# Optimization experiments

Measured on AMD Instinct MI355X. Metric: run time of the kernel, lower is better.

Reference implementation:

```python
import jax, jax.numpy as jnp
import numpy as np

B, LQ, LV = 32, 64, 128
QS, FS, BN = 512, 1024, 512

def setup_inputs() -> dict:
    key = jax.random.key(0)
    k1, k2, k3, k4, k5 = jax.random.split(key, 5)
    s = lambda n: 1.0 / np.sqrt(n)
    return {
        "phr_feats": jax.random.normal(k1, (B, LQ, QS), dtype=jnp.float32),
        "vis_feats": jax.random.normal(k2, (B, LV, FS), dtype=jnp.float32),
        "W": jax.random.uniform(k3, (BN, QS), jnp.float32, -s(QS), s(QS)),
        "U": jax.random.uniform(k4, (BN, FS), jnp.float32, -s(FS), s(FS)),
        "b": jnp.ones((BN,), dtype=jnp.float32),
        "w": jax.random.uniform(k5, (1, BN), jnp.float32, -s(BN), s(BN)),
    }

def reference(phr_feats, vis_feats, W, U, b, w):
    # Wh: [B,Lq,BN], Uv: [B,Lv,BN]
    Wh = jnp.einsum('bqd,nd->bqn', phr_feats, W)
    Uv = jnp.einsum('bvf,nf->bvn', vis_feats, U)
    # broadcast add + tanh: [B,Lq,Lv,BN]
    t = jnp.tanh(Wh[:, :, None, :] + Uv[:, None, :, :] + b)
    energies = jnp.einsum('bqvn,n->bqv', t, w[0])  # squeeze(-1)
    weights = jax.nn.softmax(energies, axis=2)
    aligned = jnp.einsum('bqv,bvf->bqf', weights, vis_feats)
    semantic_group_feats = jnp.concatenate([phr_feats, aligned], axis=2)
    return (semantic_group_feats, weights, energies)
```

## Files before the change

### kernel.cpp

```cpp
#include <hip/hip_runtime.h>

#define NB  32
#define NLQ 64
#define NLV 128
#define NQS 512
#define NFS 1024
#define NBN 512
#define CC  2.8853900817779268f

typedef float  floatx4 __attribute__((ext_vector_type(4)));
typedef __bf16 bf16x8  __attribute__((ext_vector_type(8)));
typedef unsigned short us;

__device__ __forceinline__ us f2bf(float f) {
    unsigned int u = __float_as_uint(f);
    u += 0x7fffu + ((u >> 16) & 1u);
    return (us)(u >> 16);
}
__device__ __forceinline__ unsigned int pktrunc(float lo, float hi) {
    return __builtin_amdgcn_perm(__float_as_uint(hi), __float_as_uint(lo), 0x07060302u);
}
__device__ __forceinline__ float blo(unsigned int u) {
    return __uint_as_float(u << 16);
}
__device__ __forceinline__ float bhi(unsigned int u) {
    return __uint_as_float(u & 0xffff0000u);
}

__device__ __forceinline__ void gemm64(
    us* As, us* Bs,
    const float* __restrict__ A, const float* __restrict__ Bt,
    const float* __restrict__ bias,
    float* __restrict__ whYp, us* __restrict__ uvYTp,
    int K, int bx, int by,
    float* __restrict__ sgf, us* __restrict__ visbT)
{
    const int tid  = threadIdx.x;
    const int m0   = bx * 64;
    const int n0   = by * 64;
    const int wave = tid >> 6;
    const int lane = tid & 63;
    const int wm   = (wave >> 1) * 32;
    const int wn   = (wave & 1) * 32;
    const int srow = tid >> 2;
    const int sk   = (tid & 3) * 8;
    const int fm   = lane & 15;
    const int fko  = (lane >> 4) * 8;

    floatx4 acc[2][2] = {};
    const float* ag = A  + (size_t)(m0 + srow) * K + sk;
    const float* bg = Bt + (size_t)(n0 + srow) * K + sk;

    float4 a0 = *(const float4*)(ag),     a1 = *(const float4*)(ag + 4);
    float4 b0 = *(const float4*)(bg),     b1 = *(const float4*)(bg + 4);

    for (int k0 = 0; k0 < K; k0 += 32) {
        __syncthreads();
        if (sgf) {
            float* d = sgf + (size_t)(m0 + srow) * (NQS + NFS) + k0 + sk;
            *(float4*)d       = a0;
            *(float4*)(d + 4) = a1;
        }
        uint4 av = { pktrunc(a0.x, a0.y), pktrunc(a0.z, a0.w),
                     pktrunc(a1.x, a1.y), pktrunc(a1.z, a1.w) };
        uint4 bv = { pktrunc(b0.x, b0.y), pktrunc(b0.z, b0.w),
                     pktrunc(b1.x, b1.y), pktrunc(b1.z, b1.w) };
        *(uint4*)(As + srow * 40 + sk) = av;
        *(uint4*)(Bs + srow * 40 + sk) = bv;
        const int kn = k0 + 32;
        if (kn < K) {
            a0 = *(const float4*)(ag + kn); a1 = *(const float4*)(ag + kn + 4);
            b0 = *(const float4*)(bg + kn); b1 = *(const float4*)(bg + kn + 4);
        }
        __syncthreads();
        bf16x8 am[2], bn[2];
        #pragma unroll
        for (int i = 0; i < 2; ++i)
            am[i] = *(const bf16x8*)(As + (wm + 16 * i + fm) * 40 + fko);
        #pragma unroll
        for (int j = 0; j < 2; ++j)
            bn[j] = *(const bf16x8*)(Bs + (wn + 16 * j + fm) * 40 + fko);
        #pragma unroll
        for (int i = 0; i < 2; ++i)
            #pragma unroll
            for (int j = 0; j < 2; ++j)
                acc[i][j] = __builtin_amdgcn_mfma_f32_16x16x32_bf16(am[i], bn[j], acc[i][j], 0, 0, 0);

        if (visbT) {
            const int bb = m0 >> 7, vbase = m0 & 127;
            #pragma unroll
            for (int h = 0; h < 2; ++h) {
                int idx = h * 256 + tid;
                int f   = idx >> 4;
                int v0  = (idx & 15) * 4;
                us e0 = As[(v0 + 0) * 40 + f];
                us e1 = As[(v0 + 1) * 40 + f];
                us e2 = As[(v0 + 2) * 40 + f];
                us e3 = As[(v0 + 3) * 40 + f];
                uint2 pk2 = { (unsigned int)e0 | ((unsigned int)e1 << 16),
                              (unsigned int)e2 | ((unsigned int)e3 << 16) };
                *(uint2*)(visbT + ((size_t)bb * NFS + k0 + f) * NLV + vbase + v0) = pk2;
            }
        }
    }

    const int cr = (lane >> 4) * 4;
    const int cc = lane & 15;
    if (whYp) {
        #pragma unroll
        for (int i = 0; i < 2; ++i)
            #pragma unroll
            for (int j = 0; j < 2; ++j)
                #pragma unroll
                for (int r = 0; r < 4; ++r) {
                    int gm = m0 + wm + 16 * i + cr + r;
                    int gn = n0 + wn + 16 * j + cc;
                    float v = acc[i][j][r] + bias[gn];
                    whYp[(size_t)gm * NBN + gn] = __builtin_amdgcn_exp2f(CC * v);
                }
    } else {
        #pragma unroll
        for (int i = 0; i < 2; ++i)
            #pragma unroll
            for (int j = 0; j < 2; ++j) {
                int gm0 = m0 + wm + 16 * i + cr;
                int gn  = n0 + wn + 16 * j + cc;
                int bb  = gm0 >> 7, v = gm0 & 127;
                unsigned int y0 = f2bf(__builtin_amdgcn_exp2f(CC * acc[i][j][0]));
                unsigned int y1 = f2bf(__builtin_amdgcn_exp2f(CC * acc[i][j][1]));
                unsigned int y2 = f2bf(__builtin_amdgcn_exp2f(CC * acc[i][j][2]));
                unsigned int y3 = f2bf(__builtin_amdgcn_exp2f(CC * acc[i][j][3]));
                uint2 pk2 = { y0 | (y1 << 16), y2 | (y3 << 16) };
                *(uint2*)(uvYTp + ((size_t)bb * NBN + gn) * NLV + v) = pk2;
            }
    }
}

__global__ __launch_bounds__(256) void gemm_both(
    const float* __restrict__ phr, const float* __restrict__ W,
    const float* __restrict__ bias,
    const float* __restrict__ vis, const float* __restrict__ U,
    float* __restrict__ whY, us* __restrict__ uvYT,
    float* __restrict__ out_sgf, us* __restrict__ visbT)
{
    __shared__ __align__(16) us As[64 * 40];
    __shared__ __align__(16) us Bs[64 * 40];
    int blk = blockIdx.x;
    if (blk < 256) {
        int bx = blk % 32, by = blk / 32;
        gemm64(As, Bs, phr, W, bias, whY, nullptr, NQS, bx, by,
               by == 0 ? out_sgf : nullptr, nullptr);
    } else {
        blk -= 256;
        int bx = blk % 64, by = blk / 64;
        gemm64(As, Bs, vis, U, bias, nullptr, uvYT, NFS, bx, by,
               nullptr, by == 0 ? visbT : nullptr);
    }
}

__global__ __launch_bounds__(256) void energize(
    const float* __restrict__ whY,
    const us* __restrict__ uvYT,
    const float* __restrict__ wvec,
    float* __restrict__ out_w, float* __restrict__ out_e,
    us* __restrict__ p_bf, us* __restrict__ p_lo)
{
    const float LOG2E = 1.4426950408889634f;
    int blk = blockIdx.x;
    blk = (blk & 7) * 64 + (blk >> 3);
    const int b    = blk >> 4;
    const int qq4  = blk & 15;
    const int tid  = threadIdx.x;
    const int wave = __builtin_amdgcn_readfirstlane(tid >> 6);
    const int lane = tid & 63;
    const int q0   = qq4 * 4;

    __shared__ float part[4][4][NLV];

    float4 sw0 = *(const float4*)(wvec + lane * 8);
    float4 sw1 = *(const float4*)(wvec + lane * 8 + 4);
    float sumw = sw0.x + sw0.y + sw0.z + sw0.w + sw1.x + sw1.y + sw1.z + sw1.w;
    #pragma unroll
    for (int off = 32; off; off >>= 1) sumw += __shfl_xor(sumw, off);

    const float* yqp = whY + (size_t)(b * NLQ + q0) * NBN + wave * 128;
    const float* wp  = wvec + wave * 128;
    const us*    uvp = uvYT + ((size_t)b * NBN + wave * 128) * NLV + 2 * lane;

    float acc[4][2] = {};
    #pragma unroll 2
    for (int nc = 0; nc < 128; nc += 8) {
        unsigned int yv[8];
        #pragma unroll
        for (int k = 0; k < 8; ++k)
            yv[k] = *(const unsigned int*)(uvp + (size_t)(nc + k) * NLV);
        #pragma unroll
        for (int k = 0; k < 8; ++k) {
            float x0 = blo(yv[k]), x1 = bhi(yv[k]);
            float wk = wp[nc + k];
            #pragma unroll
            for (int q = 0; q < 4; ++q) {
                float yq = yqp[q * NBN + nc + k];
                float d0 = fmaf(x0, yq, 1.f);
                float d1 = fmaf(x1, yq, 1.f);
                acc[q][0] = fmaf(wk, __builtin_amdgcn_rcpf(d0), acc[q][0]);
                acc[q][1] = fmaf(wk, __builtin_amdgcn_rcpf(d1), acc[q][1]);
            }
        }
    }
    #pragma unroll
    for (int q = 0; q < 4; ++q) {
        float2 t = { acc[q][0], acc[q][1] };
        *(float2*)&part[q][wave][2 * lane] = t;
    }
    __syncthreads();

    const int q = wave;
    float s0 = 0.f, s1 = 0.f;
    #pragma unroll
    for (int nq = 0; nq < 4; ++nq) {
        s0 += part[q][nq][2 * lane];
        s1 += part[q][nq][2 * lane + 1];
    }
    float e0 = sumw - 2.f * s0;
    float e1 = sumw - 2.f * s1;
    float m = fmaxf(e0, e1);
    #pragma unroll
    for (int off = 32; off; off >>= 1) m = fmaxf(m, __shfl_xor(m, off));
    float x0 = __builtin_amdgcn_exp2f((e0 - m) * LOG2E);
    float x1 = __builtin_amdgcn_exp2f((e1 - m) * LOG2E);
    float ss = x0 + x1;
    #pragma unroll
    for (int off = 32; off; off >>= 1) ss += __shfl_xor(ss, off);
    float inv = __builtin_amdgcn_rcpf(ss);
    float p0 = x0 * inv, p1 = x1 * inv;

    const size_t row = (size_t)(b * NLQ + q0 + q);
    float2 ep = { e0, e1 };
    float2 pp = { p0, p1 };
    *(float2*)(out_e + row * NLV + 2 * lane) = ep;
    *(float2*)(out_w + row * NLV + 2 * lane) = pp;
    unsigned int pb0 = f2bf(p0), pb1 = f2bf(p1);
    float lo0 = p0 - __uint_as_float(pb0 << 16);
    float lo1 = p1 - __uint_as_float(pb1 << 16);
    unsigned int lb0 = f2bf(lo0), lb1 = f2bf(lo1);
    *(unsigned int*)(p_bf + row * NLV + 2 * lane) = pb0 | (pb1 << 16);
    *(unsigned int*)(p_lo + row * NLV + 2 * lane) = lb0 | (lb1 << 16);
}

__global__ __launch_bounds__(256) void aligned_mfma(
    const us* __restrict__ p_bf, const us* __restrict__ p_lo,
    const us* __restrict__ visbT,
    float* __restrict__ out_sgf)
{
    int blk = blockIdx.x;
    blk = (blk & 7) * 64 + (blk >> 3);
    const int b    = blk >> 4;
    const int ft   = blk & 15;
    const int tid  = threadIdx.x;
    const int wave = tid >> 6;
    const int lane = tid & 63;
    const int wm   = (wave >> 1) * 32;
    const int wf   = (wave & 1) * 32;
    const int fm   = lane & 15;
    const int fko  = (lane >> 4) * 8;

    floatx4 acc[2][2] = {};
    const us* pA  = p_bf + ((size_t)b * NLQ + wm + fm) * NLV + fko;
    const us* pAl = p_lo + ((size_t)b * NLQ + wm + fm) * NLV + fko;
    const us* pB  = visbT + ((size_t)b * NFS + ft * 64 + wf + fm) * NLV + fko;

    #pragma unroll
    for (int ks = 0; ks < 4; ++ks) {
        bf16x8 a[2], al[2], bb[2];
        #pragma unroll
        for (int i = 0; i < 2; ++i) {
            a[i]  = *(const bf16x8*)(pA  + (size_t)i * 16 * NLV + ks * 32);
            al[i] = *(const bf16x8*)(pAl + (size_t)i * 16 * NLV + ks * 32);
        }
        #pragma unroll
        for (int j = 0; j < 2; ++j)
            bb[j] = *(const bf16x8*)(pB + (size_t)j * 16 * NLV + ks * 32);
        #pragma unroll
        for (int i = 0; i < 2; ++i)
            #pragma unroll
            for (int j = 0; j < 2; ++j) {
                acc[i][j] = __builtin_amdgcn_mfma_f32_16x16x32_bf16(a[i],  bb[j], acc[i][j], 0, 0, 0);
                acc[i][j] = __builtin_amdgcn_mfma_f32_16x16x32_bf16(al[i], bb[j], acc[i][j], 0, 0, 0);
            }
    }

    const int cr = (lane >> 4) * 4;
    const int cc = lane & 15;
    #pragma unroll
    for (int i = 0; i < 2; ++i)
        #pragma unroll
        for (int j = 0; j < 2; ++j)
            #pragma unroll
            for (int r = 0; r < 4; ++r) {
                int q = wm + 16 * i + cr + r;
                int f = ft * 64 + wf + 16 * j + cc;
                size_t row = (size_t)b * NLQ + q;
                out_sgf[row * (NQS + NFS) + NQS + f] = acc[i][j][r];
            }
}

extern "C" void kernel_launch(void* const* d_in, const int* in_sizes, int n_in,
                              void* d_out, int out_size, void* d_ws, size_t ws_size,
                              hipStream_t stream) {
    const float* phr  = (const float*)d_in[0];
    const float* vis  = (const float*)d_in[1];
    const float* W    = (const float*)d_in[2];
    const float* U    = (const float*)d_in[3];
    const float* bias = (const float*)d_in[4];
    const float* wvec = (const float*)d_in[5];

    char* ws = (char*)d_ws;
    float* whY  = (float*)ws;
    us* uvYT    = (us*)(ws + (4u << 20));
    us* visbT   = (us*)(ws + (8u << 20));
    us* p_bf    = (us*)(ws + (16u << 20));
    us* p_lo    = (us*)(ws + (16u << 20) + (512u << 10));

    float* out     = (float*)d_out;
    float* out_sgf = out;
    float* out_w   = out_sgf + (size_t)NB * NLQ * (NQS + NFS);
    float* out_e   = out_w   + (size_t)NB * NLQ * NLV;

    gemm_both<<<768, 256, 0, stream>>>(phr, W, bias, vis, U,
                                       whY, uvYT, out_sgf, visbT);
    energize<<<512, 256, 0, stream>>>(whY, uvYT, wvec, out_w, out_e, p_bf, p_lo);
    aligned_mfma<<<512, 256, 0, stream>>>(p_bf, p_lo, visbT, out_sgf);
}
```

Baseline: 128.2 us.

## Use 128x128 GEMM tiles and transpose vis into LDS inside aligned kernel

```diff
diff --git a/kernel.cpp b/kernel.cpp
--- a/kernel.cpp
+++ b/kernel.cpp
@@ -27,111 +27,105 @@
     return __uint_as_float(u & 0xffff0000u);
 }
 
-__device__ __forceinline__ void gemm64(
+__device__ __forceinline__ void gemm128(
     us* As, us* Bs,
     const float* __restrict__ A, const float* __restrict__ Bt,
     const float* __restrict__ bias,
     float* __restrict__ whYp, us* __restrict__ uvYTp,
-    int K, int bx, int by,
-    float* __restrict__ sgf, us* __restrict__ visbT)
+    int K, int bx, int by, float* __restrict__ sgf)
 {
     const int tid  = threadIdx.x;
-    const int m0   = bx * 64;
-    const int n0   = by * 64;
+    const int m0   = bx * 128;
+    const int n0   = by * 128;
     const int wave = tid >> 6;
     const int lane = tid & 63;
-    const int wm   = (wave >> 1) * 32;
-    const int wn   = (wave & 1) * 32;
-    const int srow = tid >> 2;
-    const int sk   = (tid & 3) * 8;
+    const int wm   = (wave >> 1) * 64;
+    const int wn   = (wave & 1) * 64;
+    const int srow = tid >> 1;
+    const int sk   = (tid & 1) * 16;
     const int fm   = lane & 15;
     const int fko  = (lane >> 4) * 8;
 
-    floatx4 acc[2][2] = {};
+    floatx4 acc[4][4] = {};
     const float* ag = A  + (size_t)(m0 + srow) * K + sk;
     const float* bg = Bt + (size_t)(n0 + srow) * K + sk;
 
-    float4 a0 = *(const float4*)(ag),     a1 = *(const float4*)(ag + 4);
-    float4 b0 = *(const float4*)(bg),     b1 = *(const float4*)(bg + 4);
+    float4 a[4], b[4];
+    #pragma unroll
+    for (int r = 0; r < 4; ++r) { a[r] = ((const float4*)ag)[r]; b[r] = ((const float4*)bg)[r]; }
 
     for (int k0 = 0; k0 < K; k0 += 32) {
         __syncthreads();
         if (sgf) {
             float* d = sgf + (size_t)(m0 + srow) * (NQS + NFS) + k0 + sk;
-            *(float4*)d       = a0;
-            *(float4*)(d + 4) = a1;
-        }
-        uint4 av = { pktrunc(a0.x, a0.y), pktrunc(a0.z, a0.w),
-                     pktrunc(a1.x, a1.y), pktrunc(a1.z, a1.w) };
-        uint4 bv = { pktrunc(b0.x, b0.y), pktrunc(b0.z, b0.w),
-                     pktrunc(b1.x, b1.y), pktrunc(b1.z, b1.w) };
-        *(uint4*)(As + srow * 40 + sk) = av;
-        *(uint4*)(Bs + srow * 40 + sk) = bv;
+            #pragma unroll
+            for (int r = 0; r < 4; ++r) *(float4*)(d + 4 * r) = a[r];
+        }
+        uint4 av0 = { pktrunc(a[0].x, a[0].y), pktrunc(a[0].z, a[0].w),
+                      pktrunc(a[1].x, a[1].y), pktrunc(a[1].z, a[1].w) };
+        uint4 av1 = { pktrunc(a[2].x, a[2].y), pktrunc(a[2].z, a[2].w),
+                      pktrunc(a[3].x, a[3].y), pktrunc(a[3].z, a[3].w) };
+        uint4 bv0 = { pktrunc(b[0].x, b[0].y), pktrunc(b[0].z, b[0].w),
+                      pktrunc(b[1].x, b[1].y), pktrunc(b[1].z, b[1].w) };
+        uint4 bv1 = { pktrunc(b[2].x, b[2].y), pktrunc(b[2].z, b[2].w),
+                      pktrunc(b[3].x, b[3].y), pktrunc(b[3].z, b[3].w) };
+        *(uint4*)(As + srow * 40 + sk)     = av0;
+        *(uint4*)(As + srow * 40 + sk + 8) = av1;
+        *(uint4*)(Bs + srow * 40 + sk)     = bv0;
+        *(uint4*)(Bs + srow * 40 + sk + 8) = bv1;
         const int kn = k0 + 32;
         if (kn < K) {
-            a0 = *(const float4*)(ag + kn); a1 = *(const float4*)(ag + kn + 4);
-            b0 = *(const float4*)(bg + kn); b1 = *(const float4*)(bg + kn + 4);
+            #pragma unroll
+            for (int r = 0; r < 4; ++r) {
+                a[r] = *(const float4*)(ag + kn + 4 * r);
+                b[r] = *(const float4*)(bg + kn + 4 * r);
+            }
         }
         __syncthreads();
-        bf16x8 am[2], bn[2];
-        #pragma unroll
-        for (int i = 0; i < 2; ++i)
+        bf16x8 am[4], bn[4];
+        #pragma unroll
+        for (int i = 0; i < 4; ++i)
             am[i] = *(const bf16x8*)(As + (wm + 16 * i + fm) * 40 + fko);
         #pragma unroll
-        for (int j = 0; j < 2; ++j)
+        for (int j = 0; j < 4; ++j)
             bn[j] = *(const bf16x8*)(Bs + (wn + 16 * j + fm) * 40 + fko);
         #pragma unroll
-        for (int i = 0; i < 2; ++i)
-            #pragma unroll
-            for (int j = 0; j < 2; ++j)
+        for (int i = 0; i < 4; ++i)
+            #pragma unroll
+            for (int j = 0; j < 4; ++j)
                 acc[i][j] = __builtin_amdgcn_mfma_f32_16x16x32_bf16(am[i], bn[j], acc[i][j], 0, 0, 0);
-
-        if (visbT) {
-            const int bb = m0 >> 7, vbase = m0 & 127;
-            #pragma unroll
-            for (int h = 0; h < 2; ++h) {
-                int idx = h * 256 + tid;
-                int f   = idx >> 4;
-                int v0  = (idx & 15) * 4;
-                us e0 = As[(v0 + 0) * 40 + f];
-                us e1 = As[(v0 + 1) * 40 + f];
-                us e2 = As[(v0 + 2) * 40 + f];
-                us e3 = As[(v0 + 3) * 40 + f];
-                uint2 pk2 = { (unsigned int)e0 | ((unsigned int)e1 << 16),
-                              (unsigned int)e2 | ((unsigned int)e3 << 16) };
-                *(uint2*)(visbT + ((size_t)bb * NFS + k0 + f) * NLV + vbase + v0) = pk2;
-            }
-        }
     }
 
     const int cr = (lane >> 4) * 4;
     const int cc = lane & 15;
     if (whYp) {
         #pragma unroll
-        for (int i = 0; i < 2; ++i)
-            #pragma unroll
-            for (int j = 0; j < 2; ++j)
+        for (int j = 0; j < 4; ++j) {
+            int gn = n0 + wn + 16 * j + cc;
+            float bj = bias[gn];
+            #pragma unroll
+            for (int i = 0; i < 4; ++i)
                 #pragma unroll
                 for (int r = 0; r < 4; ++r) {
                     int gm = m0 + wm + 16 * i + cr + r;
-                    int gn = n0 + wn + 16 * j + cc;
-                    float v = acc[i][j][r] + bias[gn];
-                    whYp[(size_t)gm * NBN + gn] = __builtin_amdgcn_exp2f(CC * v);
+                    whYp[(size_t)gm * NBN + gn] =
+                        __builtin_amdgcn_exp2f(CC * (acc[i][j][r] + bj));
                 }
+        }
     } else {
-        #pragma unroll
-        for (int i = 0; i < 2; ++i)
-            #pragma unroll
-            for (int j = 0; j < 2; ++j) {
-                int gm0 = m0 + wm + 16 * i + cr;
-                int gn  = n0 + wn + 16 * j + cc;
-                int bb  = gm0 >> 7, v = gm0 & 127;
+        const int bb = bx;
+        #pragma unroll
+        for (int i = 0; i < 4; ++i)
+            #pragma unroll
+            for (int j = 0; j < 4; ++j) {
+                int v0 = wm + 16 * i + cr;
+                int gn = n0 + wn + 16 * j + cc;
                 unsigned int y0 = f2bf(__builtin_amdgcn_exp2f(CC * acc[i][j][0]));
                 unsigned int y1 = f2bf(__builtin_amdgcn_exp2f(CC * acc[i][j][1]));
                 unsigned int y2 = f2bf(__builtin_amdgcn_exp2f(CC * acc[i][j][2]));
                 unsigned int y3 = f2bf(__builtin_amdgcn_exp2f(CC * acc[i][j][3]));
                 uint2 pk2 = { y0 | (y1 << 16), y2 | (y3 << 16) };
-                *(uint2*)(uvYTp + ((size_t)bb * NBN + gn) * NLV + v) = pk2;
+                *(uint2*)(uvYTp + ((size_t)bb * NBN + gn) * NLV + v0) = pk2;
             }
     }
 }
@@ -141,20 +135,19 @@
     const float* __restrict__ bias,
     const float* __restrict__ vis, const float* __restrict__ U,
     float* __restrict__ whY, us* __restrict__ uvYT,
-    float* __restrict__ out_sgf, us* __restrict__ visbT)
+    float* __restrict__ out_sgf)
 {
-    __shared__ __align__(16) us As[64 * 40];
-    __shared__ __align__(16) us Bs[64 * 40];
+    __shared__ __align__(16) us As[128 * 40];
+    __shared__ __align__(16) us Bs[128 * 40];
     int blk = blockIdx.x;
-    if (blk < 256) {
-        int bx = blk % 32, by = blk / 32;
-        gemm64(As, Bs, phr, W, bias, whY, nullptr, NQS, bx, by,
-               by == 0 ? out_sgf : nullptr, nullptr);
+    if (blk < 64) {
+        int bx = blk & 15, by = blk >> 4;
+        gemm128(As, Bs, phr, W, bias, whY, nullptr, NQS, bx, by,
+                by == 0 ? out_sgf : nullptr);
     } else {
-        blk -= 256;
-        int bx = blk % 64, by = blk / 64;
-        gemm64(As, Bs, vis, U, bias, nullptr, uvYT, NFS, bx, by,
-               nullptr, by == 0 ? visbT : nullptr);
+        blk -= 64;
+        int bx = blk & 31, by = blk >> 5;
+        gemm128(As, Bs, vis, U, bias, nullptr, uvYT, NFS, bx, by, nullptr);
     }
 }
 
@@ -250,7 +243,7 @@
 
 __global__ __launch_bounds__(256) void aligned_mfma(
     const us* __restrict__ p_bf, const us* __restrict__ p_lo,
-    const us* __restrict__ visbT,
+    const float* __restrict__ vis,
     float* __restrict__ out_sgf)
 {
     int blk = blockIdx.x;
@@ -265,14 +258,30 @@
     const int fm   = lane & 15;
     const int fko  = (lane >> 4) * 8;
 
+    __shared__ us Vs[64][136];
+
+    {
+        const int v  = tid >> 1;
+        const int fh = (tid & 1) * 32;
+        const float* vp = vis + ((size_t)b * NLV + v) * NFS + ft * 64 + fh;
+        #pragma unroll
+        for (int r = 0; r < 8; ++r) {
+            float4 x = ((const float4*)vp)[r];
+            Vs[fh + 4 * r + 0][v] = (us)(__float_as_uint(x.x) >> 16);
+            Vs[fh + 4 * r + 1][v] = (us)(__float_as_uint(x.y) >> 16);
+            Vs[fh + 4 * r + 2][v] = (us)(__float_as_uint(x.z) >> 16);
+            Vs[fh + 4 * r + 3][v] = (us)(__float_as_uint(x.w) >> 16);
+        }
+    }
+    __syncthreads();
+
     floatx4 acc[2][2] = {};
     const us* pA  = p_bf + ((size_t)b * NLQ + wm + fm) * NLV + fko;
     const us* pAl = p_lo + ((size_t)b * NLQ + wm + fm) * NLV + fko;
-    const us* pB  = visbT + ((size_t)b * NFS + ft * 64 + wf + fm) * NLV + fko;
 
     #pragma unroll
     for (int ks = 0; ks < 4; ++ks) {
-        bf16x8 a[2], al[2], bb[2];
+        bf16x8 a[2], al[2], bb2[2];
         #pragma unroll
         for (int i = 0; i < 2; ++i) {
             a[i]  = *(const bf16x8*)(pA  + (size_t)i * 16 * NLV + ks * 32);
@@ -280,13 +289,13 @@
         }
         #pragma unroll
         for (int j = 0; j < 2; ++j)
-            bb[j] = *(const bf16x8*)(pB + (size_t)j * 16 * NLV + ks * 32);
+            bb2[j] = *(const bf16x8*)&Vs[wf + 16 * j + fm][ks * 32 + fko];
         #pragma unroll
         for (int i = 0; i < 2; ++i)
             #pragma unroll
             for (int j = 0; j < 2; ++j) {
-                acc[i][j] = __builtin_amdgcn_mfma_f32_16x16x32_bf16(a[i],  bb[j], acc[i][j], 0, 0, 0);
-                acc[i][j] = __builtin_amdgcn_mfma_f32_16x16x32_bf16(al[i], bb[j], acc[i][j], 0, 0, 0);
+                acc[i][j] = __builtin_amdgcn_mfma_f32_16x16x32_bf16(a[i],  bb2[j], acc[i][j], 0, 0, 0);
+                acc[i][j] = __builtin_amdgcn_mfma_f32_16x16x32_bf16(al[i], bb2[j], acc[i][j], 0, 0, 0);
             }
     }
 
@@ -318,17 +327,15 @@
     char* ws = (char*)d_ws;
     float* whY  = (float*)ws;
     us* uvYT    = (us*)(ws + (4u << 20));
-    us* visbT   = (us*)(ws + (8u << 20));
-    us* p_bf    = (us*)(ws + (16u << 20));
-    us* p_lo    = (us*)(ws + (16u << 20) + (512u << 10));
+    us* p_bf    = (us*)(ws + (8u << 20));
+    us* p_lo    = (us*)(ws + (8u << 20) + (512u << 10));
 
     float* out     = (float*)d_out;
     float* out_sgf = out;
     float* out_w   = out_sgf + (size_t)NB * NLQ * (NQS + NFS);
     float* out_e   = out_w   + (size_t)NB * NLQ * NLV;
 
-    gemm_both<<<768, 256, 0, stream>>>(phr, W, bias, vis, U,
-                                       whY, uvYT, out_sgf, visbT);
+    gemm_both<<<192, 256, 0, stream>>>(phr, W, bias, vis, U, whY, uvYT, out_sgf);
     energize<<<512, 256, 0, stream>>>(whY, uvYT, wvec, out_w, out_e, p_bf, p_lo);
-    aligned_mfma<<<512, 256, 0, stream>>>(p_bf, p_lo, visbT, out_sgf);
-}
+    aligned_mfma<<<512, 256, 0, stream>>>(p_bf, p_lo, vis, out_sgf);
+}
```

Measured after the change: 138.0 us. +7.7%, slower.

## Build bf16 transposed vis tile in aligned kernel instead of in GEMM

Applied to the files above, without the earlier changes.

```diff
diff --git a/kernel.cpp b/kernel.cpp
--- a/kernel.cpp
+++ b/kernel.cpp
@@ -32,8 +32,7 @@
     const float* __restrict__ A, const float* __restrict__ Bt,
     const float* __restrict__ bias,
     float* __restrict__ whYp, us* __restrict__ uvYTp,
-    int K, int bx, int by,
-    float* __restrict__ sgf, us* __restrict__ visbT)
+    int K, int bx, int by, float* __restrict__ sgf)
 {
     const int tid  = threadIdx.x;
     const int m0   = bx * 64;
@@ -85,39 +84,24 @@
             #pragma unroll
             for (int j = 0; j < 2; ++j)
                 acc[i][j] = __builtin_amdgcn_mfma_f32_16x16x32_bf16(am[i], bn[j], acc[i][j], 0, 0, 0);
-
-        if (visbT) {
-            const int bb = m0 >> 7, vbase = m0 & 127;
-            #pragma unroll
-            for (int h = 0; h < 2; ++h) {
-                int idx = h * 256 + tid;
-                int f   = idx >> 4;
-                int v0  = (idx & 15) * 4;
-                us e0 = As[(v0 + 0) * 40 + f];
-                us e1 = As[(v0 + 1) * 40 + f];
-                us e2 = As[(v0 + 2) * 40 + f];
-                us e3 = As[(v0 + 3) * 40 + f];
-                uint2 pk2 = { (unsigned int)e0 | ((unsigned int)e1 << 16),
-                              (unsigned int)e2 | ((unsigned int)e3 << 16) };
-                *(uint2*)(visbT + ((size_t)bb * NFS + k0 + f) * NLV + vbase + v0) = pk2;
-            }
-        }
     }
 
     const int cr = (lane >> 4) * 4;
     const int cc = lane & 15;
     if (whYp) {
         #pragma unroll
-        for (int i = 0; i < 2; ++i)
-            #pragma unroll
-            for (int j = 0; j < 2; ++j)
+        for (int j = 0; j < 2; ++j) {
+            int gn = n0 + wn + 16 * j + cc;
+            float bj = bias[gn];
+            #pragma unroll
+            for (int i = 0; i < 2; ++i)
                 #pragma unroll
                 for (int r = 0; r < 4; ++r) {
                     int gm = m0 + wm + 16 * i + cr + r;
-                    int gn = n0 + wn + 16 * j + cc;
-                    float v = acc[i][j][r] + bias[gn];
-                    whYp[(size_t)gm * NBN + gn] = __builtin_amdgcn_exp2f(CC * v);
+                    whYp[(size_t)gm * NBN + gn] =
+                        __builtin_amdgcn_exp2f(CC * (acc[i][j][r] + bj));
                 }
+        }
     } else {
         #pragma unroll
         for (int i = 0; i < 2; ++i)
@@ -125,13 +109,13 @@
             for (int j = 0; j < 2; ++j) {
                 int gm0 = m0 + wm + 16 * i + cr;
                 int gn  = n0 + wn + 16 * j + cc;
-                int bb  = gm0 >> 7, v = gm0 & 127;
+                int bb  = gm0 >> 7, v0 = gm0 & 127;
                 unsigned int y0 = f2bf(__builtin_amdgcn_exp2f(CC * acc[i][j][0]));
                 unsigned int y1 = f2bf(__builtin_amdgcn_exp2f(CC * acc[i][j][1]));
                 unsigned int y2 = f2bf(__builtin_amdgcn_exp2f(CC * acc[i][j][2]));
                 unsigned int y3 = f2bf(__builtin_amdgcn_exp2f(CC * acc[i][j][3]));
                 uint2 pk2 = { y0 | (y1 << 16), y2 | (y3 << 16) };
-                *(uint2*)(uvYTp + ((size_t)bb * NBN + gn) * NLV + v) = pk2;
+                *(uint2*)(uvYTp + ((size_t)bb * NBN + gn) * NLV + v0) = pk2;
             }
     }
 }
@@ -141,7 +125,7 @@
     const float* __restrict__ bias,
     const float* __restrict__ vis, const float* __restrict__ U,
     float* __restrict__ whY, us* __restrict__ uvYT,
-    float* __restrict__ out_sgf, us* __restrict__ visbT)
+    float* __restrict__ out_sgf)
 {
     __shared__ __align__(16) us As[64 * 40];
     __shared__ __align__(16) us Bs[64 * 40];
@@ -149,12 +133,11 @@
     if (blk < 256) {
         int bx = blk % 32, by = blk / 32;
         gemm64(As, Bs, phr, W, bias, whY, nullptr, NQS, bx, by,
-               by == 0 ? out_sgf : nullptr, nullptr);
+               by == 0 ? out_sgf : nullptr);
     } else {
         blk -= 256;
         int bx = blk % 64, by = blk / 64;
-        gemm64(As, Bs, vis, U, bias, nullptr, uvYT, NFS, bx, by,
-               nullptr, by == 0 ? visbT : nullptr);
+        gemm64(As, Bs, vis, U, bias, nullptr, uvYT, NFS, bx, by, nullptr);
     }
 }
 
@@ -250,7 +233,7 @@
 
 __global__ __launch_bounds__(256) void aligned_mfma(
     const us* __restrict__ p_bf, const us* __restrict__ p_lo,
-    const us* __restrict__ visbT,
+    const float* __restrict__ vis,
     float* __restrict__ out_sgf)
 {
     int blk = blockIdx.x;
@@ -265,14 +248,30 @@
     const int fm   = lane & 15;
     const int fko  = (lane >> 4) * 8;
 
+    __shared__ us Vs[64][136];
+
+    {
+        const int v  = tid >> 1;
+        const int fh = (tid & 1) * 32;
+        const float* vp = vis + ((size_t)b * NLV + v) * NFS + ft * 64 + fh;
+        #pragma unroll
+        for (int r = 0; r < 8; ++r) {
+            float4 x = ((const float4*)vp)[r];
+            Vs[fh + 4 * r + 0][v] = (us)(__float_as_uint(x.x) >> 16);
+            Vs[fh + 4 * r + 1][v] = (us)(__float_as_uint(x.y) >> 16);
+            Vs[fh + 4 * r + 2][v] = (us)(__float_as_uint(x.z) >> 16);
+            Vs[fh + 4 * r + 3][v] = (us)(__float_as_uint(x.w) >> 16);
+        }
+    }
+    __syncthreads();
+
     floatx4 acc[2][2] = {};
     const us* pA  = p_bf + ((size_t)b * NLQ + wm + fm) * NLV + fko;
     const us* pAl = p_lo + ((size_t)b * NLQ + wm + fm) * NLV + fko;
-    const us* pB  = visbT + ((size_t)b * NFS + ft * 64 + wf + fm) * NLV + fko;
 
     #pragma unroll
     for (int ks = 0; ks < 4; ++ks) {
-        bf16x8 a[2], al[2], bb[2];
+        bf16x8 a[2], al[2], bb2[2];
         #pragma unroll
         for (int i = 0; i < 2; ++i) {
             a[i]  = *(const bf16x8*)(pA  + (size_t)i * 16 * NLV + ks * 32);
@@ -280,13 +279,13 @@
         }
         #pragma unroll
         for (int j = 0; j < 2; ++j)
-            bb[j] = *(const bf16x8*)(pB + (size_t)j * 16 * NLV + ks * 32);
+            bb2[j] = *(const bf16x8*)&Vs[wf + 16 * j + fm][ks * 32 + fko];
         #pragma unroll
         for (int i = 0; i < 2; ++i)
             #pragma unroll
             for (int j = 0; j < 2; ++j) {
-                acc[i][j] = __builtin_amdgcn_mfma_f32_16x16x32_bf16(a[i],  bb[j], acc[i][j], 0, 0, 0);
-                acc[i][j] = __builtin_amdgcn_mfma_f32_16x16x32_bf16(al[i], bb[j], acc[i][j], 0, 0, 0);
+                acc[i][j] = __builtin_amdgcn_mfma_f32_16x16x32_bf16(a[i],  bb2[j], acc[i][j], 0, 0, 0);
+                acc[i][j] = __builtin_amdgcn_mfma_f32_16x16x32_bf16(al[i], bb2[j], acc[i][j], 0, 0, 0);
             }
     }
 
@@ -318,17 +317,15 @@
     char* ws = (char*)d_ws;
     float* whY  = (float*)ws;
     us* uvYT    = (us*)(ws + (4u << 20));
-    us* visbT   = (us*)(ws + (8u << 20));
-    us* p_bf    = (us*)(ws + (16u << 20));
-    us* p_lo    = (us*)(ws + (16u << 20) + (512u << 10));
+    us* p_bf    = (us*)(ws + (8u << 20));
+    us* p_lo    = (us*)(ws + (8u << 20) + (512u << 10));
 
     float* out     = (float*)d_out;
     float* out_sgf = out;
     float* out_w   = out_sgf + (size_t)NB * NLQ * (NQS + NFS);
     float* out_e   = out_w   + (size_t)NB * NLQ * NLV;
 
-    gemm_both<<<768, 256, 0, stream>>>(phr, W, bias, vis, U,
-                                       whY, uvYT, out_sgf, visbT);
+    gemm_both<<<768, 256, 0, stream>>>(phr, W, bias, vis, U, whY, uvYT, out_sgf);
     energize<<<512, 256, 0, stream>>>(whY, uvYT, wvec, out_w, out_e, p_bf, p_lo);
-    aligned_mfma<<<512, 256, 0, stream>>>(p_bf, p_lo, visbT, out_sgf);
-}
+    aligned_mfma<<<512, 256, 0, stream>>>(p_bf, p_lo, vis, out_sgf);
+}
```

After: 126.3 us. About the same (-1.5%).
